# Kernel tuning notes

Hardware: AMD Instinct MI355X
Metric: run time of the kernel (lower is better)

Reference implementation:

```python
import jax, jax.numpy as jnp
import numpy as np

N_NODES = 100000
N_EDGES = 3200000


def setup_inputs() -> dict:
    key = jax.random.key(0)
    ks = jax.random.split(key, 8)
    x = jax.random.normal(ks[0], (N_NODES, 128), dtype=jnp.float32)
    edge_index = jax.random.randint(ks[1], (2, N_EDGES), 0, N_NODES, dtype=jnp.int64)
    edge_weight = jax.random.uniform(ks[2], (N_EDGES,), dtype=jnp.float32)
    W1 = jax.random.normal(ks[3], (128, 32), dtype=jnp.float32) * (1.0 / np.sqrt(128))
    b1 = jnp.zeros((32,), dtype=jnp.float32)
    W2 = jax.random.normal(ks[4], (32, 16), dtype=jnp.float32) * (1.0 / np.sqrt(32))
    b2 = jnp.zeros((16,), dtype=jnp.float32)
    Wfc = jax.random.normal(ks[5], (16, 1), dtype=jnp.float32) * (1.0 / np.sqrt(16))
    bfc = jnp.zeros((1,), dtype=jnp.float32)
    return {"x": x, "edge_index": edge_index, "edge_weight": edge_weight,
            "W1": W1, "b1": b1, "W2": W2, "b2": b2, "Wfc": Wfc, "bfc": bfc}


def _gcn_norm(edge_index, edge_weight, num_nodes):
    # PyG gcn_norm: add self-loops (weight 1), sym-normalize by in-degree of target (col)
    row, col = edge_index[0], edge_index[1]
    loop = jnp.arange(num_nodes, dtype=row.dtype)
    row_f = jnp.concatenate([row, loop])
    col_f = jnp.concatenate([col, loop])
    w_f = jnp.concatenate([edge_weight, jnp.ones((num_nodes,), edge_weight.dtype)])
    deg = jax.ops.segment_sum(w_f, col_f, num_segments=num_nodes)
    dinv = jnp.where(deg > 0, deg ** -0.5, 0.0)
    norm_w = dinv[row_f] * w_f * dinv[col_f]  # [E+N]
    return row_f, col_f, norm_w


def _gcn_conv(x, row_f, col_f, norm_w, W, b, num_nodes):
    h = x @ W                      # transform first (in->out dims)
    msg = h[row_f] * norm_w[:, None]  # gather source features, scale by edge norm
    out = jax.ops.segment_sum(msg, col_f, num_segments=num_nodes)  # scatter-add to targets
    return out + b


def reference(x, edge_index, edge_weight, W1, b1, W2, b2, Wfc, bfc):
    N = x.shape[0]
    row_f, col_f, norm_w = _gcn_norm(edge_index, edge_weight, N)
    h = jax.nn.leaky_relu(_gcn_conv(x, row_f, col_f, norm_w, W1, b1, N))
    # dropout is identity in eval mode; norm=False skips GraphNorm
    h = jax.nn.leaky_relu(_gcn_conv(h, row_f, col_f, norm_w, W2, b2, N))
    return h @ Wfc + bfc  # [N, 1]
```

## Files before the change

### kernel.cpp

```cpp
#include <hip/hip_runtime.h>
#include <hip/hip_fp16.h>

#define N_NODES 100000
#define N_EDGES 3200000
#define BSHIFT 7
#define BSIZE 128
#define NB ((N_NODES + BSIZE - 1) / BSIZE)
#define CAP 4736
#define ROWBITS 17
#define ROWMASK ((1 << ROWBITS) - 1)
#define EPB 8192
#define SC_GRID ((N_EDGES + EPB - 1) / EPB)


__global__ void k_detect(const unsigned* __restrict__ w, int* __restrict__ flag) {
    __shared__ unsigned s[256];
    unsigned v = 0;
    for (int t = threadIdx.x; t < 4096; t += 256) v |= w[2 * t + 1];
    s[threadIdx.x] = v;
    __syncthreads();
    for (int off = 128; off > 0; off >>= 1) {
        if (threadIdx.x < (unsigned)off) s[threadIdx.x] |= s[threadIdx.x + off];
        __syncthreads();
    }
    if (threadIdx.x == 0) flag[0] = (s[0] == 0) ? 1 : 0;
}

__device__ __forceinline__ void load_edge(const unsigned* __restrict__ e, int f, int E,
                                          int i, int& r, int& c) {
    if (f) { r = (int)e[2 * i]; c = (int)e[2 * E + 2 * i]; }
    else   { r = (int)e[i];     c = (int)e[E + i]; }
}


__global__ __launch_bounds__(512) void k_scatter(const unsigned* __restrict__ eidx,
                                                 const int* __restrict__ flag,
                                                 const float* __restrict__ ew,
                                                 int* __restrict__ gcursor,
                                                 int2* __restrict__ bstage, int E, int n) {
    __shared__ int lcnt[NB];
    __shared__ int lbase[NB];
    int tid = threadIdx.x;
    for (int i = tid; i < NB; i += 512) lcnt[i] = 0;
    __syncthreads();
    int f = flag[0];
    int base = blockIdx.x * EPB;
    int lim = min(EPB, E - base);
    for (int i = tid; i < lim; i += 512) {
        int r, c;
        load_edge(eidx, f, E, base + i, r, c);
        if ((unsigned)r < (unsigned)n && (unsigned)c < (unsigned)n)
            atomicAdd(&lcnt[c >> BSHIFT], 1);
    }
    __syncthreads();
    for (int i = tid; i < NB; i += 512)
        if (lcnt[i]) lbase[i] = atomicAdd(&gcursor[i], lcnt[i]);
    __syncthreads();
    for (int i = tid; i < lim; i += 512) {
        int e = base + i;
        int r, c;
        load_edge(eidx, f, E, e, r, c);
        if ((unsigned)r < (unsigned)n && (unsigned)c < (unsigned)n) {
            int b = c >> BSHIFT, off = c & (BSIZE - 1);
            int pos = atomicAdd(&lbase[b], 1);
            if (pos < CAP)
                bstage[(size_t)b * CAP + pos] =
                    make_int2((off << ROWBITS) | r, __float_as_int(ew[e]));
        }
    }
}


__global__ __launch_bounds__(256) void k_passb(const int* __restrict__ gcursor,
                                               int2* __restrict__ erw,
                                               int* __restrict__ start,
                                               int* __restrict__ end,
                                               float* __restrict__ dinv, int n) {
    __shared__ int2  se[CAP];
    __shared__ int   cnt[256];
    __shared__ float wsm[BSIZE];
    __shared__ int   cur[BSIZE];
    int tid = threadIdx.x;
    int b = blockIdx.x;
    int n0 = b << BSHIFT;
    int nn = min(BSIZE, n - n0);
    size_t bb = (size_t)b * CAP;
    int cntE = min(gcursor[b], CAP);
    cnt[tid] = 0;
    if (tid < BSIZE) wsm[tid] = 0.f;
    __syncthreads();
    for (int e = tid; e < cntE; e += 256) {
        int2 kv = erw[bb + e];
        se[e] = kv;
        int off = kv.x >> ROWBITS;
        atomicAdd(&cnt[off], 1);
        atomicAdd(&wsm[off], __int_as_float(kv.y));
    }
    __syncthreads();
    int v = cnt[tid];
    for (int o = 1; o < 256; o <<= 1) {
        int t = (tid >= o) ? cnt[tid - o] : 0;
        __syncthreads();
        cnt[tid] += t;
        __syncthreads();
    }
    int excl = cnt[tid] - v;
    if (tid < nn) {
        start[n0 + tid] = (int)bb + excl;
        end[n0 + tid]   = (int)bb + excl + v;
        dinv[n0 + tid]  = 1.0f / sqrtf(1.0f + wsm[tid]);
    }
    if (tid < BSIZE) cur[tid] = excl;
    __syncthreads();
    for (int e = tid; e < cntE; e += 256) {
        int2 kv = se[e];
        int off = kv.x >> ROWBITS;
        int p = atomicAdd(&cur[off], 1);
        erw[bb + p] = make_int2(kv.x & ROWMASK, kv.y);
    }
}


__global__ __launch_bounds__(256) void k_gemm1(const float* __restrict__ x,
                                               const float* __restrict__ W1,
                                               const float* __restrict__ dinv,
                                               __half* __restrict__ g1, int n) {
    __shared__ float W1s[128 * 32];
    __shared__ float xs[8][128];
    int tid = threadIdx.x;
    for (int i = tid; i < 1024; i += 256)
        *reinterpret_cast<float4*>(W1s + 4 * i) = reinterpret_cast<const float4*>(W1)[i];
    int node0 = blockIdx.x * 8;
    {
        int ln = tid >> 5, ii = tid & 31;
        int node = node0 + ln;
        float4 vv = make_float4(0.f, 0.f, 0.f, 0.f);
        if (node < n) vv = reinterpret_cast<const float4*>(x)[node * 32 + ii];
        *reinterpret_cast<float4*>(&xs[ln][4 * ii]) = vv;
    }
    __syncthreads();
    int ln = tid >> 5;
    int kk = tid & 31;
    int node = node0 + ln;
    if (node < n) {
        float acc = 0.f;
#pragma unroll
        for (int i = 0; i < 128; ++i) acc += xs[ln][i] * W1s[i * 32 + kk];
        g1[node * 32 + kk] = __float2half(dinv[node] * acc);
    }
}


__global__ __launch_bounds__(256) void k_agg1(const __half* __restrict__ g,
                                              const int* __restrict__ start,
                                              const int* __restrict__ end,
                                              const int2* __restrict__ erw,
                                              const float* __restrict__ dinv,
                                              const float* __restrict__ b1,
                                              float* __restrict__ h, int n) {
    int wid = (blockIdx.x * 256 + threadIdx.x) >> 6;
    int l = threadIdx.x & 63;
    if (wid >= n) return;
    int slot = l >> 3;
    int cg   = l & 7;
    int s = start[wid], en = end[wid];
    float4 acc = make_float4(0.f, 0.f, 0.f, 0.f);
    for (int e0 = s; e0 < en; e0 += 8) {
        int e = e0 + slot;
        bool ok = e < en;
        int2 rw = erw[ok ? e : s];
        float w = ok ? __int_as_float(rw.y) : 0.f;
        float2 raw = *reinterpret_cast<const float2*>(g + ((size_t)rw.x << 5) + (cg << 2));
        __half2 h01 = *reinterpret_cast<const __half2*>(&raw.x);
        __half2 h23 = *reinterpret_cast<const __half2*>(&raw.y);
        float2 f01 = __half22float2(h01), f23 = __half22float2(h23);
        acc.x += w * f01.x; acc.y += w * f01.y;
        acc.z += w * f23.x; acc.w += w * f23.y;
    }
#pragma unroll
    for (int m = 8; m <= 32; m <<= 1) {
        acc.x += __shfl_xor(acc.x, m);
        acc.y += __shfl_xor(acc.y, m);
        acc.z += __shfl_xor(acc.z, m);
        acc.w += __shfl_xor(acc.w, m);
    }
    if (slot == 0) {
        float2 raw = *reinterpret_cast<const float2*>(g + ((size_t)wid << 5) + (cg << 2));
        __half2 h01 = *reinterpret_cast<const __half2*>(&raw.x);
        __half2 h23 = *reinterpret_cast<const __half2*>(&raw.y);
        float2 f01 = __half22float2(h01), f23 = __half22float2(h23);
        float di = dinv[wid];
        float4 b = *reinterpret_cast<const float4*>(b1 + (cg << 2));
        float4 v;
        v.x = di * (acc.x + f01.x) + b.x;
        v.y = di * (acc.y + f01.y) + b.y;
        v.z = di * (acc.z + f23.x) + b.z;
        v.w = di * (acc.w + f23.y) + b.w;
        v.x = v.x > 0.f ? v.x : 0.01f * v.x;
        v.y = v.y > 0.f ? v.y : 0.01f * v.y;
        v.z = v.z > 0.f ? v.z : 0.01f * v.z;
        v.w = v.w > 0.f ? v.w : 0.01f * v.w;
        *reinterpret_cast<float4*>(h + ((size_t)wid << 5) + (cg << 2)) = v;
    }
}


__global__ __launch_bounds__(256) void k_gemm2(const float* __restrict__ h1,
                                               const float* __restrict__ W2,
                                               const float* __restrict__ dinv,
                                               __half* __restrict__ g2, int n) {
    __shared__ float W2s[32 * 16];
    int tid = threadIdx.x;
    for (int i = tid; i < 32 * 16; i += 256) W2s[i] = W2[i];
    __syncthreads();
    int t = blockIdx.x * 256 + tid;
    if (t < n * 16) {
        int node = t >> 4, j = t & 15;
        float acc = 0.f;
#pragma unroll
        for (int k = 0; k < 32; ++k) acc += h1[node * 32 + k] * W2s[k * 16 + j];
        g2[t] = __float2half(dinv[node] * acc);
    }
}


__global__ __launch_bounds__(256) void k_agg2(const __half* __restrict__ g2,
                                              const int* __restrict__ start,
                                              const int* __restrict__ end,
                                              const int2* __restrict__ erw,
                                              const float* __restrict__ dinv,
                                              const float* __restrict__ b2,
                                              const float* __restrict__ Wfc,
                                              const float* __restrict__ bfc,
                                              float* __restrict__ out, int n) {
    int wid = (blockIdx.x * 256 + threadIdx.x) >> 6;
    int l = threadIdx.x & 63;
    if (wid >= n) return;
    int slot = l >> 2;
    int cg   = l & 3;
    int s = start[wid], en = end[wid];
    float4 acc = make_float4(0.f, 0.f, 0.f, 0.f);
    for (int e0 = s; e0 < en; e0 += 16) {
        int e = e0 + slot;
        bool ok = e < en;
        int2 rw = erw[ok ? e : s];
        float w = ok ? __int_as_float(rw.y) : 0.f;
        float2 raw = *reinterpret_cast<const float2*>(g2 + ((size_t)rw.x << 4) + (cg << 2));
        __half2 h01 = *reinterpret_cast<const __half2*>(&raw.x);
        __half2 h23 = *reinterpret_cast<const __half2*>(&raw.y);
        float2 f01 = __half22float2(h01), f23 = __half22float2(h23);
        acc.x += w * f01.x; acc.y += w * f01.y;
        acc.z += w * f23.x; acc.w += w * f23.y;
    }
#pragma unroll
    for (int m = 4; m <= 32; m <<= 1) {
        acc.x += __shfl_xor(acc.x, m);
        acc.y += __shfl_xor(acc.y, m);
        acc.z += __shfl_xor(acc.z, m);
        acc.w += __shfl_xor(acc.w, m);
    }
    float2 raw = *reinterpret_cast<const float2*>(g2 + ((size_t)wid << 4) + (cg << 2));
    __half2 h01 = *reinterpret_cast<const __half2*>(&raw.x);
    __half2 h23 = *reinterpret_cast<const __half2*>(&raw.y);
    float2 f01 = __half22float2(h01), f23 = __half22float2(h23);
    float di = dinv[wid];
    float4 b = *reinterpret_cast<const float4*>(b2 + (cg << 2));
    float4 wf = *reinterpret_cast<const float4*>(Wfc + (cg << 2));
    float4 v;
    v.x = di * (acc.x + f01.x) + b.x;
    v.y = di * (acc.y + f01.y) + b.y;
    v.z = di * (acc.z + f23.x) + b.z;
    v.w = di * (acc.w + f23.y) + b.w;
    v.x = v.x > 0.f ? v.x : 0.01f * v.x;
    v.y = v.y > 0.f ? v.y : 0.01f * v.y;
    v.z = v.z > 0.f ? v.z : 0.01f * v.z;
    v.w = v.w > 0.f ? v.w : 0.01f * v.w;
    float p = v.x * wf.x + v.y * wf.y + v.z * wf.z + v.w * wf.w;
    p += __shfl_xor(p, 1);
    p += __shfl_xor(p, 2);
    if (l == 0) out[wid] = p + bfc[0];
}

extern "C" void kernel_launch(void* const* d_in, const int* in_sizes, int n_in,
                              void* d_out, int out_size, void* d_ws, size_t ws_size,
                              hipStream_t stream) {
    const float*    x    = (const float*)d_in[0];
    const unsigned* eidx = (const unsigned*)d_in[1];
    const float*    ew   = (const float*)d_in[2];
    const float*    W1   = (const float*)d_in[3];
    const float*    b1   = (const float*)d_in[4];
    const float*    W2   = (const float*)d_in[5];
    const float*    b2   = (const float*)d_in[6];
    const float*    Wfc  = (const float*)d_in[7];
    const float*    bfc  = (const float*)d_in[8];
    float* out = (float*)d_out;

    const int N = N_NODES;
    const int E = N_EDGES;

    char* ws = (char*)d_ws;
    int*    flag    = (int*)ws;
    int*    gcursor = (int*)(ws + 4096);
    int*    start   = (int*)(ws + 64u * 1024);
    int*    end     = (int*)(ws + 512u * 1024);
    float*  dinv    = (float*)(ws + 1024u * 1024);
    int2*   erw     = (int2*)(ws + 2u * 1024 * 1024);
    __half* g1h     = (__half*)(ws + 32u * 1024 * 1024);
    float*  h1      = (float*)(ws + 39u * 1024 * 1024);
    __half* g2h     = (__half*)(ws + 52u * 1024 * 1024);

    k_detect<<<1, 256, 0, stream>>>(eidx, flag);

    hipMemsetAsync(gcursor, 0, (size_t)NB * sizeof(int), stream);
    k_scatter<<<SC_GRID, 512, 0, stream>>>(eidx, flag, ew, gcursor, erw, E, N);
    k_passb<<<NB, 256, 0, stream>>>(gcursor, erw, start, end, dinv, N);

    k_gemm1<<<(N + 7) / 8, 256, 0, stream>>>(x, W1, dinv, g1h, N);
    {
        int blocks = (int)(((long long)N * 64 + 255) / 256);
        k_agg1<<<blocks, 256, 0, stream>>>(g1h, start, end, erw, dinv, b1, h1, N);
    }

    k_gemm2<<<(N * 16 + 255) / 256, 256, 0, stream>>>(h1, W2, dinv, g2h, N);
    {
        int blocks = (int)(((long long)N * 64 + 255) / 256);
        k_agg2<<<blocks, 256, 0, stream>>>(g2h, start, end, erw, dinv, b2, Wfc, bfc, out, N);
    }
}
```

Baseline: 373.5 us.

## Replace global-atomic bucket scatter with per-block local sort and transposed count tables

The edge scatter no longer reserves slots with global atomics per bucket. Each block now sorts its 8192 edges locally by destination bucket in LDS and writes them out contiguously, along with per-block count and offset tables. The second pass gathers each bucket's segments from all blocks using a prefix sum over those tables. This removes scattered global writes and global atomic contention, but adds a per-bucket serial gather loop over 391 source segments, whose load balance and latency are uncertain. The workspace is also reorganised so the staging buffer is reused for later feature buffers.

```diff
diff --git a/kernel.cpp b/kernel.cpp
--- a/kernel.cpp
+++ b/kernel.cpp
@@ -10,7 +10,7 @@
 #define ROWBITS 17
 #define ROWMASK ((1 << ROWBITS) - 1)
 #define EPB 8192
-#define SC_GRID ((N_EDGES + EPB - 1) / EPB)
+#define NBLOCKS ((N_EDGES + EPB - 1) / EPB)
 
 
 __global__ void k_detect(const unsigned* __restrict__ w, int* __restrict__ flag) {
@@ -36,47 +36,83 @@
 __global__ __launch_bounds__(512) void k_scatter(const unsigned* __restrict__ eidx,
                                                  const int* __restrict__ flag,
                                                  const float* __restrict__ ew,
-                                                 int* __restrict__ gcursor,
-                                                 int2* __restrict__ bstage, int E, int n) {
-    __shared__ int lcnt[NB];
-    __shared__ int lbase[NB];
+                                                 int2* __restrict__ staged,
+                                                 int* __restrict__ cntT,
+                                                 int* __restrict__ offT, int E, int n) {
+    __shared__ int2 se[EPB];
+    __shared__ int  hist[NB];
+    __shared__ int  bpos[NB];
+    __shared__ int  s2[512];
     int tid = threadIdx.x;
-    for (int i = tid; i < NB; i += 512) lcnt[i] = 0;
+    int blk = blockIdx.x;
+    for (int i = tid; i < NB; i += 512) hist[i] = 0;
     __syncthreads();
     int f = flag[0];
-    int base = blockIdx.x * EPB;
+    int base = blk * EPB;
     int lim = min(EPB, E - base);
-    for (int i = tid; i < lim; i += 512) {
-        int r, c;
-        load_edge(eidx, f, E, base + i, r, c);
-        if ((unsigned)r < (unsigned)n && (unsigned)c < (unsigned)n)
-            atomicAdd(&lcnt[c >> BSHIFT], 1);
-    }
-    __syncthreads();
-    for (int i = tid; i < NB; i += 512)
-        if (lcnt[i]) lbase[i] = atomicAdd(&gcursor[i], lcnt[i]);
-    __syncthreads();
-    for (int i = tid; i < lim; i += 512) {
-        int e = base + i;
-        int r, c;
-        load_edge(eidx, f, E, e, r, c);
-        if ((unsigned)r < (unsigned)n && (unsigned)c < (unsigned)n) {
-            int b = c >> BSHIFT, off = c & (BSIZE - 1);
-            int pos = atomicAdd(&lbase[b], 1);
-            if (pos < CAP)
-                bstage[(size_t)b * CAP + pos] =
-                    make_int2((off << ROWBITS) | r, __float_as_int(ew[e]));
+    int rr[16], cc[16];
+    float wv[16];
+#pragma unroll
+    for (int k = 0; k < 16; ++k) {
+        int i = k * 512 + tid;
+        rr[k] = -1; cc[k] = 0; wv[k] = 0.f;
+        if (i < lim) {
+            int r, c;
+            load_edge(eidx, f, E, base + i, r, c);
+            if ((unsigned)r < (unsigned)n && (unsigned)c < (unsigned)n) {
+                rr[k] = r; cc[k] = c; wv[k] = ew[base + i];
+            }
         }
     }
-}
-
-
-__global__ __launch_bounds__(256) void k_passb(const int* __restrict__ gcursor,
+#pragma unroll
+    for (int k = 0; k < 16; ++k)
+        if (rr[k] >= 0) atomicAdd(&hist[cc[k] >> BSHIFT], 1);
+    __syncthreads();
+    int c0 = (2 * tid < NB) ? hist[2 * tid] : 0;
+    int c1 = (2 * tid + 1 < NB) ? hist[2 * tid + 1] : 0;
+    s2[tid] = c0 + c1;
+    __syncthreads();
+    for (int o = 1; o < 512; o <<= 1) {
+        int t = (tid >= o) ? s2[tid - o] : 0;
+        __syncthreads();
+        s2[tid] += t;
+        __syncthreads();
+    }
+    int cbase = s2[tid] - (c0 + c1);
+    if (2 * tid < NB) bpos[2 * tid] = cbase;
+    if (2 * tid + 1 < NB) bpos[2 * tid + 1] = cbase + c0;
+    __syncthreads();
+    for (int b = tid; b < NB; b += 512) {
+        cntT[(size_t)blk * NB + b] = hist[b];
+        offT[(size_t)blk * NB + b] = bpos[b];
+    }
+    __syncthreads();
+#pragma unroll
+    for (int k = 0; k < 16; ++k) {
+        if (rr[k] >= 0) {
+            int b = cc[k] >> BSHIFT, off = cc[k] & (BSIZE - 1);
+            int pos = atomicAdd(&bpos[b], 1);
+            se[pos] = make_int2((off << ROWBITS) | rr[k], __float_as_int(wv[k]));
+        }
+    }
+    __syncthreads();
+    for (int i = tid; i < lim; i += 512)
+        staged[(size_t)blk * EPB + i] = se[i];
+}
+
+
+__global__ __launch_bounds__(256) void k_passb(const int2* __restrict__ staged,
+                                               const int* __restrict__ cntT,
+                                               const int* __restrict__ offT,
                                                int2* __restrict__ erw,
                                                int* __restrict__ start,
                                                int* __restrict__ end,
                                                float* __restrict__ dinv, int n) {
     __shared__ int2  se[CAP];
+    __shared__ int   rcnt[NBLOCKS + 1];
+    __shared__ int   roff[NBLOCKS + 1];
+    __shared__ int   rdst[NBLOCKS + 1];
+    __shared__ int   s2[256];
     __shared__ int   cnt[256];
     __shared__ float wsm[BSIZE];
     __shared__ int   cur[BSIZE];
@@ -85,16 +121,43 @@
     int n0 = b << BSHIFT;
     int nn = min(BSIZE, n - n0);
     size_t bb = (size_t)b * CAP;
-    int cntE = min(gcursor[b], CAP);
+    for (int j = tid; j < NBLOCKS; j += 256) {
+        rcnt[j] = cntT[(size_t)j * NB + b];
+        roff[j] = offT[(size_t)j * NB + b];
+    }
+    __syncthreads();
+    int c0 = (2 * tid < NBLOCKS) ? rcnt[2 * tid] : 0;
+    int c1 = (2 * tid + 1 < NBLOCKS) ? rcnt[2 * tid + 1] : 0;
+    s2[tid] = c0 + c1;
+    __syncthreads();
+    for (int o = 1; o < 256; o <<= 1) {
+        int t = (tid >= o) ? s2[tid - o] : 0;
+        __syncthreads();
+        s2[tid] += t;
+        __syncthreads();
+    }
+    int cbase = s2[tid] - (c0 + c1);
+    if (2 * tid < NBLOCKS) rdst[2 * tid] = cbase;
+    if (2 * tid + 1 < NBLOCKS) rdst[2 * tid + 1] = cbase + c0;
+    if (tid == 255) rdst[NBLOCKS] = s2[255];
     cnt[tid] = 0;
     if (tid < BSIZE) wsm[tid] = 0.f;
     __syncthreads();
+    int cntE = min(rdst[NBLOCKS], CAP);
+    for (int j = tid; j < NBLOCKS; j += 256) {
+        int len = rcnt[j];
+        int dst = rdst[j];
+        size_t src = (size_t)j * EPB + roff[j];
+        for (int i = 0; i < len; ++i) {
+            int d = dst + i;
+            if (d < CAP) se[d] = staged[src + i];
+        }
+    }
+    __syncthreads();
     for (int e = tid; e < cntE; e += 256) {
-        int2 kv = erw[bb + e];
-        se[e] = kv;
-        int off = kv.x >> ROWBITS;
+        int off = se[e].x >> ROWBITS;
         atomicAdd(&cnt[off], 1);
-        atomicAdd(&wsm[off], __int_as_float(kv.y));
+        atomicAdd(&wsm[off], __int_as_float(se[e].y));
     }
     __syncthreads();
     int v = cnt[tid];
@@ -299,21 +362,22 @@
     const int E = N_EDGES;
 
     char* ws = (char*)d_ws;
-    int*    flag    = (int*)ws;
-    int*    gcursor = (int*)(ws + 4096);
-    int*    start   = (int*)(ws + 64u * 1024);
-    int*    end     = (int*)(ws + 512u * 1024);
-    float*  dinv    = (float*)(ws + 1024u * 1024);
-    int2*   erw     = (int2*)(ws + 2u * 1024 * 1024);
-    __half* g1h     = (__half*)(ws + 32u * 1024 * 1024);
-    float*  h1      = (float*)(ws + 39u * 1024 * 1024);
-    __half* g2h     = (__half*)(ws + 52u * 1024 * 1024);
+    int*    flag   = (int*)ws;
+    int*    start  = (int*)(ws + 64u * 1024);
+    int*    end    = (int*)(ws + 512u * 1024);
+    float*  dinv   = (float*)(ws + 1024u * 1024);
+    int*    cntT   = (int*)(ws + 1536u * 1024);
+    int*    offT   = (int*)(ws + 2816u * 1024);
+    int2*   staged = (int2*)(ws + 4u * 1024 * 1024);
+    int2*   erw    = (int2*)(ws + 30u * 1024 * 1024);
+    __half* g1h    = (__half*)(ws + 4u * 1024 * 1024);
+    float*  h1     = (float*)(ws + 11u * 1024 * 1024);
+    __half* g2h    = (__half*)(ws + 24u * 1024 * 1024);
 
     k_detect<<<1, 256, 0, stream>>>(eidx, flag);
 
-    hipMemsetAsync(gcursor, 0, (size_t)NB * sizeof(int), stream);
-    k_scatter<<<SC_GRID, 512, 0, stream>>>(eidx, flag, ew, gcursor, erw, E, N);
-    k_passb<<<NB, 256, 0, stream>>>(gcursor, erw, start, end, dinv, N);
+    k_scatter<<<NBLOCKS, 512, 0, stream>>>(eidx, flag, ew, staged, cntT, offT, E, N);
+    k_passb<<<NB, 256, 0, stream>>>(staged, cntT, offT, erw, start, end, dinv, N);
 
     k_gemm1<<<(N + 7) / 8, 256, 0, stream>>>(x, W1, dinv, g1h, N);
     {
```

After: 381.8 us. 1.02x slower.
